# Optimization experiments

Measured on AMD Instinct MI355X. Metric: run time of the kernel, lower is better.

Reference implementation:

```python
import jax, jax.numpy as jnp
import numpy as np

GROUPS = 32
EPS = 1e-5


def group_norm(x, gamma, beta):
    # x: [N, C, H, W]
    N, C, H, W = x.shape
    xg = x.reshape(N, GROUPS, C // GROUPS, H, W)
    mean = xg.mean(axis=(2, 3, 4), keepdims=True)
    var = xg.var(axis=(2, 3, 4), keepdims=True)
    xg = (xg - mean) * jax.lax.rsqrt(var + EPS)
    x = xg.reshape(N, C, H, W)
    return x * gamma[None, :, None, None] + beta[None, :, None, None]


def conv1x1(x, w, b):
    # x: [N, C, H, W], w: [O, C], b: [O]
    return jnp.einsum('nchw,oc->nohw', x, w) + b[None, :, None, None]


def setup_inputs() -> dict:
    key = jax.random.key(0)
    ks = jax.random.split(key, 12)
    N, C, H, W = 16, 512, 32, 32
    s = 1.0 / np.sqrt(C)
    inp = {
        'x': jax.random.normal(ks[0], (N, C, H, W), dtype=jnp.float32),
        'gamma': jnp.ones((C,), dtype=jnp.float32),
        'beta': jnp.zeros((C,), dtype=jnp.float32),
        'wq': jax.random.normal(ks[1], (C, C), dtype=jnp.float32) * s,
        'bq': jnp.zeros((C,), dtype=jnp.float32),
        'wk': jax.random.normal(ks[2], (C, C), dtype=jnp.float32) * s,
        'bk': jnp.zeros((C,), dtype=jnp.float32),
        'wv': jax.random.normal(ks[3], (C, C), dtype=jnp.float32) * s,
        'bv': jnp.zeros((C,), dtype=jnp.float32),
        'wo': jax.random.normal(ks[4], (C, C), dtype=jnp.float32) * s,
        'bo': jnp.zeros((C,), dtype=jnp.float32),
    }
    return inp


def reference(x, gamma, beta, wq, bq, wk, bk, wv, bv, wo, bo):
    N, C, H, W = x.shape
    h = group_norm(x, gamma, beta)
    q = conv1x1(h, wq, bq)  # [N, C, H, W]
    k = conv1x1(h, wk, bk)
    v = conv1x1(h, wv, bv)
    # flatten spatial dims to sequence of length S = H*W
    q = q.reshape(N, C, H * W).transpose(0, 2, 1)  # [N, S, C]
    k = k.reshape(N, C, H * W)                     # [N, C, S]
    v = v.reshape(N, C, H * W).transpose(0, 2, 1)  # [N, S, C]
    scale = C ** (-0.5)
    w = jnp.einsum('nsc,nct->nst', q, k) * scale   # [N, S, S]
    w = jax.nn.softmax(w, axis=-1)
    h = jnp.einsum('nst,ntc->nsc', w, v)           # [N, S, C]
    h = h.reshape(N, H, W, C).transpose(0, 3, 1, 2)  # [N, C, H, W]
    h = conv1x1(h, wo, bo)
    return x + h
```

## Files before the change

### kernel.cpp

```cpp
#include <hip/hip_runtime.h>

#define GROUPS 32
#define EPS 1e-5f

typedef unsigned short u16;
typedef __bf16 bf16x8 __attribute__((ext_vector_type(8)));
typedef float f32x4 __attribute__((ext_vector_type(4)));

__device__ __forceinline__ u16 f2bf(float f) {
  unsigned x = __builtin_bit_cast(unsigned, f);
  x += 0x7FFFu + ((x >> 16) & 1u);
  return (u16)(x >> 16);
}
__device__ __forceinline__ float bf2f(u16 u) {
  unsigned x = ((unsigned)u) << 16;
  return __builtin_bit_cast(float, x);
}

__device__ __forceinline__ void gload_lds16(const void* g, void* l) {
  __builtin_amdgcn_global_load_lds(
      (const __attribute__((address_space(1))) void*)g,
      (__attribute__((address_space(3))) void*)l, 16, 0, 0);
}

__global__ __launch_bounds__(256) void cvt_kernel(
    const float* __restrict__ wq, const float* __restrict__ wk,
    const float* __restrict__ wv, const float* __restrict__ wo,
    u16* __restrict__ Wqk, u16* __restrict__ Wv, u16* __restrict__ Wo,
    int n) {
  int i = (blockIdx.x * 256 + threadIdx.x) * 4;
  if (i >= n) return;
  const float* src;
  u16* dst;
  switch (blockIdx.y) {
    case 0: src = wq; dst = Wqk; break;
    case 1: src = wk; dst = Wqk + n; break;
    case 2: src = wv; dst = Wv; break;
    default: src = wo; dst = Wo; break;
  }
  float4 v = *(const float4*)&src[i];
  ushort4 o;
  o.x = f2bf(v.x); o.y = f2bf(v.y); o.z = f2bf(v.z); o.w = f2bf(v.w);
  *(ushort4*)&dst[i] = o;
}

__global__ __launch_bounds__(256) void biascat_kernel(
    const float* __restrict__ bq, const float* __restrict__ bk,
    float* __restrict__ bqk, int C) {
  int i = blockIdx.x * 256 + threadIdx.x;
  if (i < C) bqk[i] = bq[i];
  else if (i < 2 * C) bqk[i] = bk[i - C];
}

__global__ __launch_bounds__(256) void groupnorm_kernel(
    const float* __restrict__ x, const float* __restrict__ gamma,
    const float* __restrict__ beta, u16* __restrict__ HT, int C, int S) {
  const int cpg = C / GROUPS;
  __shared__ float xs[16 * 1024];
  __shared__ float rs[4], rss[4];
  int n = blockIdx.x / GROUPS;
  int g = blockIdx.x % GROUPS;
  const float* xb = x + ((size_t)n * C + (size_t)g * cpg) * S;
  int tid = threadIdx.x;
  int cnt = cpg * S;
  float s = 0.f, ss = 0.f;
  for (int i = tid * 4; i < cnt; i += 256 * 4) {
    float4 v = *(const float4*)&xb[i];
    *(float4*)&xs[i] = v;
    s += v.x + v.y + v.z + v.w;
    ss += v.x * v.x + v.y * v.y + v.z * v.z + v.w * v.w;
  }
  for (int o = 32; o > 0; o >>= 1) {
    s += __shfl_xor(s, o);
    ss += __shfl_xor(ss, o);
  }
  int wave = tid >> 6, lane = tid & 63;
  if (lane == 0) { rs[wave] = s; rss[wave] = ss; }
  __syncthreads();
  float S1 = rs[0] + rs[1] + rs[2] + rs[3];
  float S2 = rss[0] + rss[1] + rss[2] + rss[3];
  float mean = S1 / (float)cnt;
  float var = S2 / (float)cnt - mean * mean;
  float rstd = rsqrtf(var + EPS);
  float gm[16], bt[16];
#pragma unroll
  for (int c = 0; c < 16; ++c) {
    float gmv = gamma[g * cpg + c] * rstd;
    gm[c] = gmv;
    bt[c] = beta[g * cpg + c] - mean * gmv;
  }
  for (int i = 0; i < S; i += 256) {
    int sp = i + tid;
    u16 outv[16];
#pragma unroll
    for (int c = 0; c < 16; ++c) {
      float h = xs[c * 1024 + sp] * gm[c] + bt[c];
      outv[c] = f2bf(h);
    }
    u16* dst = HT + ((size_t)n * S + sp) * C + g * cpg;
    *(int4*)dst = *(int4*)&outv[0];
    *(int4*)&dst[8] = *(int4*)&outv[8];
  }
}

__global__ __launch_bounds__(512, 4) void gemm256x128_kernel(
    const u16* __restrict__ A, long lda, long strideA,
    const u16* __restrict__ B, long ldb, long strideB,
    void* __restrict__ Out, long ldo, long strideO, int out_fp32,
    const float* __restrict__ bias, int bias_mode,
    float scale, const float* __restrict__ residual, int K, int nbx, int nby) {
  __shared__ u16 lds[24576];
  u16* As0 = lds;
  u16* Bs0 = lds + 8192;
  u16* As1 = lds + 12288;
  u16* Bs1 = lds + 20480;

  int tid = threadIdx.x;
  int wave = tid >> 6, lane = tid & 63;
  int wr = wave >> 1, wc = wave & 1;
  int l15 = lane & 15, l4 = lane >> 4;

  int nwg = gridDim.x;
  int orig = blockIdx.x;
  int swz = ((nwg & 7) == 0) ? (orig & 7) * (nwg >> 3) + (orig >> 3) : orig;
  int tilesPB = nbx * nby;
  int z = swz / tilesPB, rem = swz % tilesPB;
  int bx = rem % nbx, by = rem / nbx;

  const u16* Ab = A + (long)z * strideA + (long)by * 256 * lda;
  const u16* Bb = B + (long)z * strideB + (long)bx * 128 * ldb;

  auto STAGE = [&](u16* Ad, u16* Bd, int kt) {
#pragma unroll
    for (int i = 0; i < 2; ++i) {
      int c = i * 512 + tid;
      int l = c >> 3, p = c & 7;
      int q = p ^ (l & 7);
      int row = 2 * l + (q >> 2);
      long koff = (long)kt * 32 + (q & 3) * 8;
      int lbase = (i * 512 + wave * 64) * 8;
      gload_lds16(Ab + (long)row * lda + koff, Ad + lbase);
    }
    {
      int c = tid;
      int l = c >> 3, p = c & 7;
      int q = p ^ (l & 7);
      int row = 2 * l + (q >> 2);
      long koff = (long)kt * 32 + (q & 3) * 8;
      int lbase = (wave * 64) * 8;
      gload_lds16(Bb + (long)row * ldb + koff, Bd + lbase);
    }
  };

  f32x4 acc[4][4] = {};

  auto COMPUTE = [&](const u16* Asrc, const u16* Bsrc) {
    bf16x8 af[4], bfr[4];
#pragma unroll
    for (int m = 0; m < 4; ++m) {
      int R = wr * 64 + m * 16 + l15;
      int line = R >> 1;
      int p = ((R & 1) * 4 + l4) ^ (line & 7);
      af[m] = *(const bf16x8*)&Asrc[line * 64 + p * 8];
    }
#pragma unroll
    for (int n = 0; n < 4; ++n) {
      int R = wc * 64 + n * 16 + l15;
      int line = R >> 1;
      int p = ((R & 1) * 4 + l4) ^ (line & 7);
      bfr[n] = *(const bf16x8*)&Bsrc[line * 64 + p * 8];
    }
#pragma unroll
    for (int m = 0; m < 4; ++m)
#pragma unroll
      for (int n = 0; n < 4; ++n)
        acc[m][n] = __builtin_amdgcn_mfma_f32_16x16x32_bf16(
            af[m], bfr[n], acc[m][n], 0, 0, 0);
  };

  int NT = K >> 5;
  u16 *Ar = As0, *Br = Bs0, *Aw = As1, *Bw = Bs1;

  STAGE(Ar, Br, 0);
  asm volatile("s_waitcnt vmcnt(0)" ::: "memory");
  __builtin_amdgcn_sched_barrier(0);
  __builtin_amdgcn_s_barrier();
  __builtin_amdgcn_sched_barrier(0);

  for (int t = 0; t < NT - 1; ++t) {
    STAGE(Aw, Bw, t + 1);
    COMPUTE(Ar, Br);
    asm volatile("s_waitcnt vmcnt(0)" ::: "memory");
    __builtin_amdgcn_sched_barrier(0);
    __builtin_amdgcn_s_barrier();
    __builtin_amdgcn_sched_barrier(0);
    u16* tp;
    tp = Ar; Ar = Aw; Aw = tp;
    tp = Br; Br = Bw; Bw = tp;
  }
  COMPUTE(Ar, Br);

  long orow0 = (long)by * 256 + wr * 64;
  long ocol0 = (long)bx * 128 + wc * 64;
#pragma unroll
  for (int m = 0; m < 4; ++m) {
#pragma unroll
    for (int n = 0; n < 4; ++n) {
#pragma unroll
      for (int r = 0; r < 4; ++r) {
        long row = orow0 + m * 16 + l4 * 4 + r;
        long col = ocol0 + n * 16 + l15;
        float v = acc[m][n][r] * scale;
        if (bias_mode == 1) v += bias[row];
        else if (bias_mode == 2) v += bias[col];
        long off = (long)z * strideO + row * ldo + col;
        if (residual) v += residual[off];
        if (out_fp32) ((float*)Out)[off] = v;
        else ((u16*)Out)[off] = f2bf(v);
      }
    }
  }
}

__global__ __launch_bounds__(256) void softmax_kernel(u16* __restrict__ P, int S) {
  size_t row = blockIdx.x;
  u16* p = P + row * (size_t)S;
  int tid = threadIdx.x;
  ushort4 u = *(const ushort4*)&p[tid * 4];
  float v0 = bf2f(u.x), v1 = bf2f(u.y), v2 = bf2f(u.z), v3 = bf2f(u.w);
  float m = fmaxf(fmaxf(v0, v1), fmaxf(v2, v3));
  for (int o = 32; o > 0; o >>= 1) m = fmaxf(m, __shfl_xor(m, o));
  __shared__ float redm[4], reds[4];
  int wave = tid >> 6, lane = tid & 63;
  if (lane == 0) redm[wave] = m;
  __syncthreads();
  m = fmaxf(fmaxf(redm[0], redm[1]), fmaxf(redm[2], redm[3]));
  float e0 = __expf(v0 - m), e1 = __expf(v1 - m);
  float e2 = __expf(v2 - m), e3 = __expf(v3 - m);
  float s = e0 + e1 + e2 + e3;
  for (int o = 32; o > 0; o >>= 1) s += __shfl_xor(s, o);
  if (lane == 0) reds[wave] = s;
  __syncthreads();
  s = reds[0] + reds[1] + reds[2] + reds[3];
  float inv = 1.f / s;
  ushort4 o4;
  o4.x = f2bf(e0 * inv); o4.y = f2bf(e1 * inv);
  o4.z = f2bf(e2 * inv); o4.w = f2bf(e3 * inv);
  *(ushort4*)&p[tid * 4] = o4;
}

extern "C" void kernel_launch(void* const* d_in, const int* in_sizes, int n_in,
                              void* d_out, int out_size, void* d_ws, size_t ws_size,
                              hipStream_t stream) {
  const float* x = (const float*)d_in[0];
  const float* gamma = (const float*)d_in[1];
  const float* beta = (const float*)d_in[2];
  const float* wq = (const float*)d_in[3];
  const float* bq = (const float*)d_in[4];
  const float* wk = (const float*)d_in[5];
  const float* bk = (const float*)d_in[6];
  const float* wv = (const float*)d_in[7];
  const float* bv = (const float*)d_in[8];
  const float* wo = (const float*)d_in[9];
  const float* bo = (const float*)d_in[10];

  const int C = 512, S = 1024;
  const int N = in_sizes[0] / (C * S);
  const long SC = (long)S * C;
  const long S2C = (long)S * 2 * C;
  const long SS = (long)S * S;
  const int CC = C * C;

  char* ws = (char*)d_ws;
  const size_t MB = 1024 * 1024;
  u16* HT = (u16*)(ws + 0 * MB);
  u16* QKT = (u16*)(ws + 16 * MB);
  u16* Vb = (u16*)(ws + 48 * MB);
  u16* P = (u16*)(ws + 64 * MB);
  u16* Wqk = (u16*)(ws + 96 * MB);
  u16* Wv = Wqk + 2 * CC;
  u16* Wo = Wv + CC;
  float* bqk = (float*)(Wo + CC);
  u16* H2T = HT;

  cvt_kernel<<<dim3(CC / 1024, 4), 256, 0, stream>>>(wq, wk, wv, wo, Wqk, Wv, Wo, CC);
  biascat_kernel<<<4, 256, 0, stream>>>(bq, bk, bqk, C);
  groupnorm_kernel<<<N * GROUPS, 256, 0, stream>>>(x, gamma, beta, HT, C, S);

  const float scl = 1.0f / sqrtf((float)C);

  gemm256x128_kernel<<<dim3((S / 256) * (2 * C / 128) * N), 512, 0, stream>>>(
      HT, C, SC, Wqk, C, 0, QKT, 2 * C, S2C, 0, bqk, 2, 1.f, nullptr, C,
      2 * C / 128, S / 256);
  gemm256x128_kernel<<<dim3((C / 256) * (S / 128) * N), 512, 0, stream>>>(
      Wv, C, 0, HT, C, SC, Vb, S, SC, 0, bv, 1, 1.f, nullptr, C,
      S / 128, C / 256);
  gemm256x128_kernel<<<dim3((S / 256) * (S / 128) * N), 512, 0, stream>>>(
      QKT, 2 * C, S2C, QKT + C, 2 * C, S2C, P, S, SS, 0, nullptr, 0, scl,
      nullptr, C, S / 128, S / 256);
  softmax_kernel<<<N * S, 256, 0, stream>>>(P, S);
  gemm256x128_kernel<<<dim3((S / 256) * (C / 128) * N), 512, 0, stream>>>(
      P, S, SS, Vb, S, SC, H2T, C, SC, 0, nullptr, 0, 1.f, nullptr, S,
      C / 128, S / 256);
  gemm256x128_kernel<<<dim3((C / 256) * (S / 128) * N), 512, 0, stream>>>(
      Wo, C, 0, H2T, C, SC, d_out, S, SC, 1, bo, 1, 1.f, x, C,
      S / 128, C / 256);
}
```

Before: 200.8 us.

## Fuse softmax normalization into the PV GEMM A-operand load, keep row stats only

The softmax kernel now only computes per-row max and reciprocal sum and writes these small stat arrays instead of rewriting the full score matrix. The P·V GEMM applies exp(x-max)*inv to the A fragments after reading them from LDS, before the MFMAs. This removes a full read-modify-write pass over the N×S×S bf16 score matrix. In exchange, each P·V tile recomputes exponentials for every A fragment (repeated across column tiles) and adds VALU work inside the GEMM inner loop. The block-to-batch swizzle mapping is also changed so that consecutive groups of 8 blocks map to different batch entries.

```diff
diff --git a/kernel.cpp b/kernel.cpp
--- a/kernel.cpp
+++ b/kernel.cpp
@@ -5,6 +5,7 @@
 
 typedef unsigned short u16;
 typedef __bf16 bf16x8 __attribute__((ext_vector_type(8)));
+typedef unsigned short u16x8 __attribute__((ext_vector_type(8)));
 typedef float f32x4 __attribute__((ext_vector_type(4)));
 
 __device__ __forceinline__ u16 f2bf(float f) {
@@ -108,7 +109,9 @@
     const u16* __restrict__ B, long ldb, long strideB,
     void* __restrict__ Out, long ldo, long strideO, int out_fp32,
     const float* __restrict__ bias, int bias_mode,
-    float scale, const float* __restrict__ residual, int K, int nbx, int nby) {
+    float scale, const float* __restrict__ residual, int K, int nbx, int nby,
+    const float* __restrict__ smax, const float* __restrict__ sinv,
+    long sstr) {
   __shared__ u16 lds[24576];
   u16* As0 = lds;
   u16* Bs0 = lds + 8192;
@@ -120,15 +123,34 @@
   int wr = wave >> 1, wc = wave & 1;
   int l15 = lane & 15, l4 = lane >> 4;
 
-  int nwg = gridDim.x;
   int orig = blockIdx.x;
-  int swz = ((nwg & 7) == 0) ? (orig & 7) * (nwg >> 3) + (orig >> 3) : orig;
   int tilesPB = nbx * nby;
-  int z = swz / tilesPB, rem = swz % tilesPB;
+  int nz = gridDim.x / tilesPB;
+  int z, rem;
+  if ((nz & 7) == 0) {
+    int e = orig & 7, j = orig >> 3;
+    z = e + 8 * (j / tilesPB);
+    rem = j % tilesPB;
+  } else {
+    int swz = ((gridDim.x & 7) == 0)
+                  ? (orig & 7) * (gridDim.x >> 3) + (orig >> 3) : orig;
+    z = swz / tilesPB; rem = swz % tilesPB;
+  }
   int bx = rem % nbx, by = rem / nbx;
 
   const u16* Ab = A + (long)z * strideA + (long)by * 256 * lda;
   const u16* Bb = B + (long)z * strideB + (long)bx * 128 * ldb;
+
+  float fmx[4], fiv[4];
+  bool dosm = (smax != nullptr);
+  if (dosm) {
+#pragma unroll
+    for (int m = 0; m < 4; ++m) {
+      long gr = (long)z * sstr + (long)by * 256 + wr * 64 + m * 16 + l15;
+      fmx[m] = smax[gr];
+      fiv[m] = sinv[gr];
+    }
+  }
 
   auto STAGE = [&](u16* Ad, u16* Bd, int kt) {
 #pragma unroll
@@ -162,6 +184,18 @@
       int line = R >> 1;
       int p = ((R & 1) * 4 + l4) ^ (line & 7);
       af[m] = *(const bf16x8*)&Asrc[line * 64 + p * 8];
+    }
+    if (dosm) {
+#pragma unroll
+      for (int m = 0; m < 4; ++m) {
+        u16x8 t = __builtin_bit_cast(u16x8, af[m]);
+#pragma unroll
+        for (int e = 0; e < 8; ++e) {
+          float f = __expf(bf2f(t[e]) - fmx[m]) * fiv[m];
+          t[e] = f2bf(f);
+        }
+        af[m] = __builtin_bit_cast(bf16x8, t);
+      }
     }
 #pragma unroll
     for (int n = 0; n < 4; ++n) {
@@ -222,9 +256,11 @@
   }
 }
 
-__global__ __launch_bounds__(256) void softmax_kernel(u16* __restrict__ P, int S) {
+__global__ __launch_bounds__(256) void stats_kernel(
+    const u16* __restrict__ P, float* __restrict__ smax,
+    float* __restrict__ sinv, int S) {
   size_t row = blockIdx.x;
-  u16* p = P + row * (size_t)S;
+  const u16* p = P + row * (size_t)S;
   int tid = threadIdx.x;
   ushort4 u = *(const ushort4*)&p[tid * 4];
   float v0 = bf2f(u.x), v1 = bf2f(u.y), v2 = bf2f(u.z), v3 = bf2f(u.w);
@@ -235,18 +271,15 @@
   if (lane == 0) redm[wave] = m;
   __syncthreads();
   m = fmaxf(fmaxf(redm[0], redm[1]), fmaxf(redm[2], redm[3]));
-  float e0 = __expf(v0 - m), e1 = __expf(v1 - m);
-  float e2 = __expf(v2 - m), e3 = __expf(v3 - m);
-  float s = e0 + e1 + e2 + e3;
+  float s = __expf(v0 - m) + __expf(v1 - m) + __expf(v2 - m) + __expf(v3 - m);
   for (int o = 32; o > 0; o >>= 1) s += __shfl_xor(s, o);
   if (lane == 0) reds[wave] = s;
   __syncthreads();
   s = reds[0] + reds[1] + reds[2] + reds[3];
-  float inv = 1.f / s;
-  ushort4 o4;
-  o4.x = f2bf(e0 * inv); o4.y = f2bf(e1 * inv);
-  o4.z = f2bf(e2 * inv); o4.w = f2bf(e3 * inv);
-  *(ushort4*)&p[tid * 4] = o4;
+  if (tid == 0) {
+    smax[row] = m;
+    sinv[row] = 1.f / s;
+  }
 }
 
 extern "C" void kernel_launch(void* const* d_in, const int* in_sizes, int n_in,
@@ -281,6 +314,8 @@
   u16* Wv = Wqk + 2 * CC;
   u16* Wo = Wv + CC;
   float* bqk = (float*)(Wo + CC);
+  float* smax = bqk + 2 * C;
+  float* sinv = smax + (size_t)N * S;
   u16* H2T = HT;
 
   cvt_kernel<<<dim3(CC / 1024, 4), 256, 0, stream>>>(wq, wk, wv, wo, Wqk, Wv, Wo, CC);
@@ -291,18 +326,18 @@
 
   gemm256x128_kernel<<<dim3((S / 256) * (2 * C / 128) * N), 512, 0, stream>>>(
       HT, C, SC, Wqk, C, 0, QKT, 2 * C, S2C, 0, bqk, 2, 1.f, nullptr, C,
-      2 * C / 128, S / 256);
+      2 * C / 128, S / 256, nullptr, nullptr, 0);
   gemm256x128_kernel<<<dim3((C / 256) * (S / 128) * N), 512, 0, stream>>>(
       Wv, C, 0, HT, C, SC, Vb, S, SC, 0, bv, 1, 1.f, nullptr, C,
-      S / 128, C / 256);
+      S / 128, C / 256, nullptr, nullptr, 0);
   gemm256x128_kernel<<<dim3((S / 256) * (S / 128) * N), 512, 0, stream>>>(
       QKT, 2 * C, S2C, QKT + C, 2 * C, S2C, P, S, SS, 0, nullptr, 0, scl,
-      nullptr, C, S / 128, S / 256);
-  softmax_kernel<<<N * S, 256, 0, stream>>>(P, S);
+      nullptr, C, S / 128, S / 256, nullptr, nullptr, 0);
+  stats_kernel<<<N * S, 256, 0, stream>>>(P, smax, sinv, S);
   gemm256x128_kernel<<<dim3((S / 256) * (C / 128) * N), 512, 0, stream>>>(
       P, S, SS, Vb, S, SC, H2T, C, SC, 0, nullptr, 0, 1.f, nullptr, S,
-      C / 128, S / 256);
+      C / 128, S / 256, smax, sinv, S);
   gemm256x128_kernel<<<dim3((C / 256) * (S / 128) * N), 512, 0, stream>>>(
       Wo, C, 0, H2T, C, SC, d_out, S, SC, 1, bo, 1, 1.f, x, C,
-      S / 128, C / 256);
-}
+      S / 128, C / 256, nullptr, nullptr, 0);
+}
```

Result: slower. 220.3 us (+9.7%).

## Fuse QK^T, softmax and PV into a single flash-attention kernel

Applied to the files above, without the earlier changes.

Replaces the score GEMM, the standalone softmax and the PV GEMM with one online-softmax kernel. Each block handles 32 query rows and streams K and V tiles through LDS. This removes the materialized bf16 S×S probability matrix and its repeated HBM round trips, plus two launches. The cost is many barriers per 32-wide KV step, small MFMA tiles, and every block re-reading K/V. The GEMM block swizzle is also changed to group batches across the eight XCD slots.

```diff
diff --git a/kernel.cpp b/kernel.cpp
--- a/kernel.cpp
+++ b/kernel.cpp
@@ -120,11 +120,19 @@
   int wr = wave >> 1, wc = wave & 1;
   int l15 = lane & 15, l4 = lane >> 4;
 
-  int nwg = gridDim.x;
   int orig = blockIdx.x;
-  int swz = ((nwg & 7) == 0) ? (orig & 7) * (nwg >> 3) + (orig >> 3) : orig;
   int tilesPB = nbx * nby;
-  int z = swz / tilesPB, rem = swz % tilesPB;
+  int nz = gridDim.x / tilesPB;
+  int z, rem;
+  if ((nz & 7) == 0) {
+    int e = orig & 7, j = orig >> 3;
+    z = e + 8 * (j / tilesPB);
+    rem = j % tilesPB;
+  } else {
+    int swz = ((gridDim.x & 7) == 0)
+                  ? (orig & 7) * (gridDim.x >> 3) + (orig >> 3) : orig;
+    z = swz / tilesPB; rem = swz % tilesPB;
+  }
   int bx = rem % nbx, by = rem / nbx;
 
   const u16* Ab = A + (long)z * strideA + (long)by * 256 * lda;
@@ -222,31 +230,161 @@
   }
 }
 
-__global__ __launch_bounds__(256) void softmax_kernel(u16* __restrict__ P, int S) {
-  size_t row = blockIdx.x;
-  u16* p = P + row * (size_t)S;
+__global__ __launch_bounds__(512, 4) void flash_kernel(
+    const u16* __restrict__ QKT, const u16* __restrict__ Vb,
+    u16* __restrict__ H2T, float scl) {
+  const int S = 1024, C = 512;
+  __shared__ u16 Kl[32 * 512];
+  __shared__ u16 Vl[512 * 32];
+  __shared__ float Sl[2][32][33];
+  __shared__ u16 Pl[32][40];
+  __shared__ float rowf[32];
+
   int tid = threadIdx.x;
-  ushort4 u = *(const ushort4*)&p[tid * 4];
-  float v0 = bf2f(u.x), v1 = bf2f(u.y), v2 = bf2f(u.z), v3 = bf2f(u.w);
-  float m = fmaxf(fmaxf(v0, v1), fmaxf(v2, v3));
-  for (int o = 32; o > 0; o >>= 1) m = fmaxf(m, __shfl_xor(m, o));
-  __shared__ float redm[4], reds[4];
-  int wave = tid >> 6, lane = tid & 63;
-  if (lane == 0) redm[wave] = m;
+  int w = tid >> 6, lane = tid & 63;
+  int l15 = lane & 15, l4 = lane >> 4;
+  int wm = w & 3, wh = w >> 2;
+  int sm = wm >> 1, sn = wm & 1;
+
+  int b = blockIdx.x;
+  int e = b & 7, j = b >> 3;
+  int z = e + 8 * (j >> 5);
+  int qb = j & 31;
+  int q0 = qb * 32;
+
+  const u16* Qg = QKT + (size_t)z * S * 2 * C;
+  const u16* Kg = Qg + C;
+  const u16* Vg = Vb + (size_t)z * C * S;
+  u16* Og = H2T + (size_t)z * S * C;
+
+  bf16x8 qreg[8];
+  {
+    const u16* qp = Qg + (size_t)(q0 + sm * 16 + l15) * 2 * C + wh * 256 + l4 * 8;
+#pragma unroll
+    for (int kk = 0; kk < 8; ++kk)
+      qreg[kk] = *(const bf16x8*)(qp + kk * 32);
+  }
+
+  auto STAGE_K = [&](int t0) {
+#pragma unroll
+    for (int i = 0; i < 4; ++i) {
+      int c = i * 512 + tid;
+      int row = c >> 6, p = c & 63;
+      int g = p ^ (row & 31);
+      gload_lds16(Kg + (size_t)(t0 + row) * 2 * C + g * 8,
+                  Kl + (i * 512 + w * 64) * 8);
+    }
+  };
+  auto STAGE_V = [&](int t0) {
+#pragma unroll
+    for (int i = 0; i < 4; ++i) {
+      int c = i * 512 + tid;
+      int row = c >> 2, p = c & 3;
+      int g = p ^ ((row & 3) ^ ((row >> 2) & 3));
+      gload_lds16(Vg + (size_t)row * S + t0 + g * 8,
+                  Vl + (i * 512 + w * 64) * 8);
+    }
+  };
+
+  f32x4 acc[2][4] = {};
+  float mrow = -1e30f, lrow = 0.f;
+  int r = tid >> 4, jc = (tid & 15) * 2;
+
+  STAGE_K(0);
+  asm volatile("s_waitcnt vmcnt(0)" ::: "memory");
+  __builtin_amdgcn_sched_barrier(0);
+  __builtin_amdgcn_s_barrier();
+  __builtin_amdgcn_sched_barrier(0);
+
+  for (int t0 = 0; t0 < S; t0 += 32) {
+    STAGE_V(t0);
+    f32x4 sacc = {0.f, 0.f, 0.f, 0.f};
+    int krow = sn * 16 + l15;
+#pragma unroll
+    for (int kk = 0; kk < 8; ++kk) {
+      int gl = wh * 32 + l4 + 4 * kk;
+      int p = gl ^ (krow & 31);
+      bf16x8 kf = *(const bf16x8*)&Kl[krow * 512 + p * 8];
+      sacc = __builtin_amdgcn_mfma_f32_16x16x32_bf16(qreg[kk], kf, sacc, 0, 0, 0);
+    }
+#pragma unroll
+    for (int rr = 0; rr < 4; ++rr)
+      Sl[wh][sm * 16 + l4 * 4 + rr][sn * 16 + l15] = sacc[rr];
+    __syncthreads();
+
+    float s0 = (Sl[0][r][jc] + Sl[1][r][jc]) * scl;
+    float s1 = (Sl[0][r][jc + 1] + Sl[1][r][jc + 1]) * scl;
+    float tmax = fmaxf(s0, s1);
+#pragma unroll
+    for (int o = 1; o < 16; o <<= 1) tmax = fmaxf(tmax, __shfl_xor(tmax, o));
+    float mnew = fmaxf(mrow, tmax);
+    float sc = __expf(mrow - mnew);
+    float p0 = __expf(s0 - mnew), p1 = __expf(s1 - mnew);
+    float es = p0 + p1;
+#pragma unroll
+    for (int o = 1; o < 16; o <<= 1) es += __shfl_xor(es, o);
+    lrow = lrow * sc + es;
+    mrow = mnew;
+    Pl[r][jc] = f2bf(p0);
+    Pl[r][jc + 1] = f2bf(p1);
+    if ((tid & 15) == 0) rowf[r] = sc;
+    __syncthreads();
+
+    float fsc[2][4];
+#pragma unroll
+    for (int m = 0; m < 2; ++m)
+#pragma unroll
+      for (int rr = 0; rr < 4; ++rr)
+        fsc[m][rr] = rowf[m * 16 + l4 * 4 + rr];
+#pragma unroll
+    for (int m = 0; m < 2; ++m)
+#pragma unroll
+      for (int n = 0; n < 4; ++n)
+#pragma unroll
+        for (int rr = 0; rr < 4; ++rr)
+          acc[m][n][rr] *= fsc[m][rr];
+
+    bf16x8 pf[2], vf[4];
+#pragma unroll
+    for (int m = 0; m < 2; ++m)
+      pf[m] = *(const bf16x8*)&Pl[m * 16 + l15][l4 * 8];
+#pragma unroll
+    for (int n = 0; n < 4; ++n) {
+      int crow = w * 64 + n * 16 + l15;
+      int p = l4 ^ ((crow & 3) ^ ((crow >> 2) & 3));
+      vf[n] = *(const bf16x8*)&Vl[crow * 32 + p * 8];
+    }
+    if (t0 + 32 < S) STAGE_K(t0 + 32);
+#pragma unroll
+    for (int m = 0; m < 2; ++m)
+#pragma unroll
+      for (int n = 0; n < 4; ++n)
+        acc[m][n] = __builtin_amdgcn_mfma_f32_16x16x32_bf16(
+            pf[m], vf[n], acc[m][n], 0, 0, 0);
+    asm volatile("s_waitcnt vmcnt(0)" ::: "memory");
+    __builtin_amdgcn_sched_barrier(0);
+    __builtin_amdgcn_s_barrier();
+    __builtin_amdgcn_sched_barrier(0);
+  }
+
+  if ((tid & 15) == 0) rowf[r] = 1.f / lrow;
   __syncthreads();
-  m = fmaxf(fmaxf(redm[0], redm[1]), fmaxf(redm[2], redm[3]));
-  float e0 = __expf(v0 - m), e1 = __expf(v1 - m);
-  float e2 = __expf(v2 - m), e3 = __expf(v3 - m);
-  float s = e0 + e1 + e2 + e3;
-  for (int o = 32; o > 0; o >>= 1) s += __shfl_xor(s, o);
-  if (lane == 0) reds[wave] = s;
-  __syncthreads();
-  s = reds[0] + reds[1] + reds[2] + reds[3];
-  float inv = 1.f / s;
-  ushort4 o4;
-  o4.x = f2bf(e0 * inv); o4.y = f2bf(e1 * inv);
-  o4.z = f2bf(e2 * inv); o4.w = f2bf(e3 * inv);
-  *(ushort4*)&p[tid * 4] = o4;
+  float fin[2][4];
+#pragma unroll
+  for (int m = 0; m < 2; ++m)
+#pragma unroll
+    for (int rr = 0; rr < 4; ++rr)
+      fin[m][rr] = rowf[m * 16 + l4 * 4 + rr];
+#pragma unroll
+  for (int m = 0; m < 2; ++m)
+#pragma unroll
+    for (int n = 0; n < 4; ++n)
+#pragma unroll
+      for (int rr = 0; rr < 4; ++rr) {
+        int row = q0 + m * 16 + l4 * 4 + rr;
+        int col = w * 64 + n * 16 + l15;
+        Og[(size_t)row * C + col] = f2bf(acc[m][n][rr] * fin[m][rr]);
+      }
 }
 
 extern "C" void kernel_launch(void* const* d_in, const int* in_sizes, int n_in,
@@ -268,7 +406,6 @@
   const int N = in_sizes[0] / (C * S);
   const long SC = (long)S * C;
   const long S2C = (long)S * 2 * C;
-  const long SS = (long)S * S;
   const int CC = C * C;
 
   char* ws = (char*)d_ws;
@@ -276,7 +413,6 @@
   u16* HT = (u16*)(ws + 0 * MB);
   u16* QKT = (u16*)(ws + 16 * MB);
   u16* Vb = (u16*)(ws + 48 * MB);
-  u16* P = (u16*)(ws + 64 * MB);
   u16* Wqk = (u16*)(ws + 96 * MB);
   u16* Wv = Wqk + 2 * CC;
   u16* Wo = Wv + CC;
@@ -295,13 +431,7 @@
   gemm256x128_kernel<<<dim3((C / 256) * (S / 128) * N), 512, 0, stream>>>(
       Wv, C, 0, HT, C, SC, Vb, S, SC, 0, bv, 1, 1.f, nullptr, C,
       S / 128, C / 256);
-  gemm256x128_kernel<<<dim3((S / 256) * (S / 128) * N), 512, 0, stream>>>(
-      QKT, 2 * C, S2C, QKT + C, 2 * C, S2C, P, S, SS, 0, nullptr, 0, scl,
-      nullptr, C, S / 128, S / 256);
-  softmax_kernel<<<N * S, 256, 0, stream>>>(P, S);
-  gemm256x128_kernel<<<dim3((S / 256) * (C / 128) * N), 512, 0, stream>>>(
-      P, S, SS, Vb, S, SC, H2T, C, SC, 0, nullptr, 0, 1.f, nullptr, S,
-      C / 128, S / 256);
+  flash_kernel<<<dim3(N * (S / 32)), 512, 0, stream>>>(QKT, Vb, H2T, scl);
   gemm256x128_kernel<<<dim3((C / 256) * (S / 128) * N), 512, 0, stream>>>(
       Wo, C, 0, H2T, C, SC, d_out, S, SC, 1, bo, 1, 1.f, x, C,
       S / 128, C / 256);
```

New measurement: 256.4 us. 1.28x slower.

## Merge QK and V projection GEMMs into one launch, fold bias concat into cvt

Applied to the files above, without the earlier changes.

Folds the bias-concatenation kernel into the weight conversion kernel as an extra grid row, and merges the QK and V projection GEMMs into a single launch that dispatches on block index. It also changes the tile-to-block mapping so that, when the batch count is a multiple of 8, consecutive blocks spread across batches. The aim is to cut launch overhead and the tail between the two projection GEMMs, and possibly improve cache locality across XCDs. The merged kernel mixes two tile shapes in one grid.

```diff
diff --git a/kernel.cpp b/kernel.cpp
--- a/kernel.cpp
+++ b/kernel.cpp
@@ -26,8 +26,15 @@
 __global__ __launch_bounds__(256) void cvt_kernel(
     const float* __restrict__ wq, const float* __restrict__ wk,
     const float* __restrict__ wv, const float* __restrict__ wo,
+    const float* __restrict__ bq, const float* __restrict__ bk,
     u16* __restrict__ Wqk, u16* __restrict__ Wv, u16* __restrict__ Wo,
-    int n) {
+    float* __restrict__ bqk, int n, int C) {
+  if (blockIdx.y == 4) {
+    int j = blockIdx.x * 256 + threadIdx.x;
+    if (j < C) bqk[j] = bq[j];
+    else if (j < 2 * C) bqk[j] = bk[j - C];
+    return;
+  }
   int i = (blockIdx.x * 256 + threadIdx.x) * 4;
   if (i >= n) return;
   const float* src;
@@ -42,14 +49,6 @@
   ushort4 o;
   o.x = f2bf(v.x); o.y = f2bf(v.y); o.z = f2bf(v.z); o.w = f2bf(v.w);
   *(ushort4*)&dst[i] = o;
-}
-
-__global__ __launch_bounds__(256) void biascat_kernel(
-    const float* __restrict__ bq, const float* __restrict__ bk,
-    float* __restrict__ bqk, int C) {
-  int i = blockIdx.x * 256 + threadIdx.x;
-  if (i < C) bqk[i] = bq[i];
-  else if (i < 2 * C) bqk[i] = bk[i - C];
 }
 
 __global__ __launch_bounds__(256) void groupnorm_kernel(
@@ -103,13 +102,14 @@
   }
 }
 
-__global__ __launch_bounds__(512, 4) void gemm256x128_kernel(
+__device__ __forceinline__ void gemm_body(
+    int bid, int nblk,
     const u16* __restrict__ A, long lda, long strideA,
     const u16* __restrict__ B, long ldb, long strideB,
     void* __restrict__ Out, long ldo, long strideO, int out_fp32,
     const float* __restrict__ bias, int bias_mode,
-    float scale, const float* __restrict__ residual, int K, int nbx, int nby) {
-  __shared__ u16 lds[24576];
+    float scale, const float* __restrict__ residual, int K,
+    int nbx, int nby, u16* lds) {
   u16* As0 = lds;
   u16* Bs0 = lds + 8192;
   u16* As1 = lds + 12288;
@@ -120,11 +120,17 @@
   int wr = wave >> 1, wc = wave & 1;
   int l15 = lane & 15, l4 = lane >> 4;
 
-  int nwg = gridDim.x;
-  int orig = blockIdx.x;
-  int swz = ((nwg & 7) == 0) ? (orig & 7) * (nwg >> 3) + (orig >> 3) : orig;
   int tilesPB = nbx * nby;
-  int z = swz / tilesPB, rem = swz % tilesPB;
+  int nz = nblk / tilesPB;
+  int z, rem;
+  if ((nz & 7) == 0) {
+    int e = bid & 7, j = bid >> 3;
+    z = e + 8 * (j / tilesPB);
+    rem = j % tilesPB;
+  } else {
+    int swz = ((nblk & 7) == 0) ? (bid & 7) * (nblk >> 3) + (bid >> 3) : bid;
+    z = swz / tilesPB; rem = swz % tilesPB;
+  }
   int bx = rem % nbx, by = rem / nbx;
 
   const u16* Ab = A + (long)z * strideA + (long)by * 256 * lda;
@@ -219,6 +225,34 @@
         else ((u16*)Out)[off] = f2bf(v);
       }
     }
+  }
+}
+
+__global__ __launch_bounds__(512, 4) void gemm256x128_kernel(
+    const u16* __restrict__ A, long lda, long strideA,
+    const u16* __restrict__ B, long ldb, long strideB,
+    void* __restrict__ Out, long ldo, long strideO, int out_fp32,
+    const float* __restrict__ bias, int bias_mode,
+    float scale, const float* __restrict__ residual, int K, int nbx, int nby) {
+  __shared__ u16 lds[24576];
+  gemm_body(blockIdx.x, gridDim.x, A, lda, strideA, B, ldb, strideB,
+            Out, ldo, strideO, out_fp32, bias, bias_mode, scale, residual,
+            K, nbx, nby, lds);
+}
+
+__global__ __launch_bounds__(512, 4) void projqkv_kernel(
+    const u16* __restrict__ HT, const u16* __restrict__ Wqk,
+    const u16* __restrict__ Wv, u16* __restrict__ QKT, u16* __restrict__ Vb,
+    const float* __restrict__ bqk, const float* __restrict__ bv,
+    int nQK, int C, int S) {
+  __shared__ u16 lds[24576];
+  long SC = (long)S * C, S2C = (long)S * 2 * C;
+  if ((int)blockIdx.x < nQK) {
+    gemm_body(blockIdx.x, nQK, HT, C, SC, Wqk, C, 0, QKT, 2 * C, S2C, 0,
+              bqk, 2, 1.f, nullptr, C, 2 * C / 128, S / 256, lds);
+  } else {
+    gemm_body(blockIdx.x - nQK, gridDim.x - nQK, Wv, C, 0, HT, C, SC,
+              Vb, S, SC, 0, bv, 1, 1.f, nullptr, C, S / 128, C / 256, lds);
   }
 }
 
@@ -283,18 +317,16 @@
   float* bqk = (float*)(Wo + CC);
   u16* H2T = HT;
 
-  cvt_kernel<<<dim3(CC / 1024, 4), 256, 0, stream>>>(wq, wk, wv, wo, Wqk, Wv, Wo, CC);
-  biascat_kernel<<<4, 256, 0, stream>>>(bq, bk, bqk, C);
+  cvt_kernel<<<dim3(CC / 1024, 5), 256, 0, stream>>>(
+      wq, wk, wv, wo, bq, bk, Wqk, Wv, Wo, bqk, CC, C);
   groupnorm_kernel<<<N * GROUPS, 256, 0, stream>>>(x, gamma, beta, HT, C, S);
 
   const float scl = 1.0f / sqrtf((float)C);
-
-  gemm256x128_kernel<<<dim3((S / 256) * (2 * C / 128) * N), 512, 0, stream>>>(
-      HT, C, SC, Wqk, C, 0, QKT, 2 * C, S2C, 0, bqk, 2, 1.f, nullptr, C,
-      2 * C / 128, S / 256);
-  gemm256x128_kernel<<<dim3((C / 256) * (S / 128) * N), 512, 0, stream>>>(
-      Wv, C, 0, HT, C, SC, Vb, S, SC, 0, bv, 1, 1.f, nullptr, C,
-      S / 128, C / 256);
+  const int nQK = (S / 256) * (2 * C / 128) * N;
+  const int nV = (C / 256) * (S / 128) * N;
+
+  projqkv_kernel<<<dim3(nQK + nV), 512, 0, stream>>>(
+      HT, Wqk, Wv, QKT, Vb, bqk, bv, nQK, C, S);
   gemm256x128_kernel<<<dim3((S / 256) * (S / 128) * N), 512, 0, stream>>>(
       QKT, 2 * C, S2C, QKT + C, 2 * C, S2C, P, S, SS, 0, nullptr, 0, scl,
       nullptr, C, S / 128, S / 256);
```

Measured after the change: 175.6 us. -12.6%, faster.
